# Performance work log

Measured on AMD Instinct MI355X. Metric: run time of the kernel, lower is better.

## Reference

```python
import jax, jax.numpy as jnp
import numpy as np


def setup_inputs() -> dict:
    key = jax.random.key(0)
    k1, k2, k3 = jax.random.split(key, 3)
    N, M, D, K = 8192, 8192, 512, 128
    x = jax.random.normal(k1, (N, D), dtype=jnp.float32)
    target = jax.random.normal(k2, (M, D), dtype=jnp.float32)
    W = jax.random.normal(k3, (D, K), dtype=jnp.float32) * 0.05
    return {"x": x, "target": target, "W": W}


def reference(x, target, W):
    # phi_Brenier(x): convex potential f(x) = logsumexp(x @ W)  -> [N]
    phi_b = jax.nn.logsumexp(x @ W, axis=-1)
    # phi_Kantorovich = 0.5||x||^2 - phi_Brenier  -> [N]
    x_sq = jnp.sum(x * x, axis=-1)
    phi_k = 0.5 * x_sq - phi_b
    t_sq = jnp.sum(target * target, axis=-1)
    DD = 0.5 * (x_sq[:, None] + t_sq[None, :] - 2.0 * (x @ target.T))
    # C-transform: min over source points  -> [M]
    phi_c = jnp.min(DD - phi_k[:, None], axis=0)
    # Kantorovich dual objective (scalar)
    return jnp.mean(phi_k) + jnp.mean(phi_c)
```

## Files before the change

### kernel.cpp

```cpp
#include <hip/hip_runtime.h>
#include <hip/hip_bf16.h>
#include <stdint.h>

typedef __attribute__((ext_vector_type(8))) short short8;
typedef __attribute__((ext_vector_type(4))) float f32x4;
typedef __attribute__((ext_vector_type(16))) float f32x16;
typedef __attribute__((ext_vector_type(4))) int i32x4;
typedef __attribute__((ext_vector_type(8))) int i32x8;

#define N_PTS 8192
#define M_PTS 8192
#define DIM   512
#define KDIM  128
#define BT    128
#define BKS   32

__device__ __forceinline__ unsigned fenc(float f) {
  unsigned u = __float_as_uint(f);
  return (u & 0x80000000u) ? ~u : (u | 0x80000000u);
}
__device__ __forceinline__ float fdec(unsigned k) {
  unsigned u = (k & 0x80000000u) ? (k ^ 0x80000000u) : ~k;
  return __uint_as_float(u);
}

__device__ __forceinline__ unsigned short f2bf(float f) {
  union { __hip_bfloat16 h; unsigned short u; } c;
  c.h = __float2bfloat16(f);
  return c.u;
}

__device__ __forceinline__ unsigned f2e4m3(float f) {
  unsigned u = __float_as_uint(f);
  unsigned s = (u >> 24) & 0x80;
  unsigned mag = u & 0x7fffffffu;
  unsigned r = mag + 0x0007ffffu + ((mag >> 20) & 1u);
  int e = (int)(r >> 23) - 127;
  if (e < -6) return s;
  unsigned m = (r >> 20) & 7u;
  return s | (unsigned)((e + 7) << 3) | m;
}

__device__ __forceinline__ void async_copy16(const void* g, void* l) {
  __builtin_amdgcn_global_load_lds(
      (const __attribute__((address_space(1))) void*)g,
      (__attribute__((address_space(3))) void*)l, 16, 0, 0);
}

__device__ __forceinline__ int swz_slot(int row, int slot) {
  return slot ^ ((row >> 1) & 3);
}

#define BARRIER __builtin_amdgcn_s_barrier()
#define LGKM0 do { asm volatile("s_waitcnt lgkmcnt(0)" ::: "memory"); \
                   __builtin_amdgcn_sched_barrier(0); } while (0)

__global__ __launch_bounds__(256)
void prep_all_kernel(const float* __restrict__ x, const float* __restrict__ tgt,
                     const float* __restrict__ W,
                     unsigned short* __restrict__ Xb, unsigned char* __restrict__ Xf8,
                     unsigned char* __restrict__ Tf8, unsigned short* __restrict__ WbT,
                     float* __restrict__ xsq, float* __restrict__ tsq,
                     unsigned* __restrict__ keys) {
  const int bid = blockIdx.x;
  const int tid = threadIdx.x;
  if (bid >= (N_PTS + M_PTS) / 4) {
    const int o = (bid - (N_PTS + M_PTS) / 4) * 256 + tid;
    const int k = o >> 9, d = o & 511;
    WbT[o] = f2bf(W[d * KDIM + k]);
    return;
  }
  const int gw = (bid * 256 + tid) >> 6;
  const int j = tid & 63;
  float s;
  if (gw < N_PTS) {
    const float* src = x + (size_t)gw * DIM + j * 8;
    float4 v0 = *(const float4*)src;
    float4 v1 = *(const float4*)(src + 4);
    s = v0.x * v0.x + v0.y * v0.y + v0.z * v0.z + v0.w * v0.w +
        v1.x * v1.x + v1.y * v1.y + v1.z * v1.z + v1.w * v1.w;
    unsigned short* db = Xb + (size_t)gw * DIM + j * 8;
    ushort4 ob0, ob1;
    ob0.x = f2bf(v0.x); ob0.y = f2bf(v0.y); ob0.z = f2bf(v0.z); ob0.w = f2bf(v0.w);
    ob1.x = f2bf(v1.x); ob1.y = f2bf(v1.y); ob1.z = f2bf(v1.z); ob1.w = f2bf(v1.w);
    *(ushort4*)db = ob0;
    *(ushort4*)(db + 4) = ob1;
    unsigned long long p = (unsigned long long)f2e4m3(v0.x)
        | ((unsigned long long)f2e4m3(v0.y) << 8)
        | ((unsigned long long)f2e4m3(v0.z) << 16)
        | ((unsigned long long)f2e4m3(v0.w) << 24)
        | ((unsigned long long)f2e4m3(v1.x) << 32)
        | ((unsigned long long)f2e4m3(v1.y) << 40)
        | ((unsigned long long)f2e4m3(v1.z) << 48)
        | ((unsigned long long)f2e4m3(v1.w) << 56);
    *(unsigned long long*)(Xf8 + (size_t)gw * DIM + j * 8) = p;
#pragma unroll
    for (int m = 1; m <= 32; m <<= 1) s += __shfl_xor(s, m);
    if (j == 0) xsq[gw] = s;
  } else {
    const int tr = gw - N_PTS;
    const float* src = tgt + (size_t)tr * DIM + j * 8;
    float4 v0 = *(const float4*)src;
    float4 v1 = *(const float4*)(src + 4);
    s = v0.x * v0.x + v0.y * v0.y + v0.z * v0.z + v0.w * v0.w +
        v1.x * v1.x + v1.y * v1.y + v1.z * v1.z + v1.w * v1.w;
    unsigned long long p = (unsigned long long)f2e4m3(v0.x)
        | ((unsigned long long)f2e4m3(v0.y) << 8)
        | ((unsigned long long)f2e4m3(v0.z) << 16)
        | ((unsigned long long)f2e4m3(v0.w) << 24)
        | ((unsigned long long)f2e4m3(v1.x) << 32)
        | ((unsigned long long)f2e4m3(v1.y) << 40)
        | ((unsigned long long)f2e4m3(v1.z) << 48)
        | ((unsigned long long)f2e4m3(v1.w) << 56);
    *(unsigned long long*)(Tf8 + (size_t)tr * DIM + j * 8) = p;
#pragma unroll
    for (int m = 1; m <= 32; m <<= 1) s += __shfl_xor(s, m);
    if (j == 0) { tsq[tr] = s; keys[tr] = 0xFFFFFFFFu; }
  }
}

__global__ __launch_bounds__(256)
void phi_b_kernel(const short* __restrict__ Xb, const short* __restrict__ WbT,
                  float* __restrict__ phi_b) {
  __shared__ __align__(16) short As[BT * BKS];
  __shared__ __align__(16) short Bs[BT * BKS];
  __shared__ __align__(16) float lg[128][136];

  const int tid = threadIdx.x;
  const int wave = tid >> 6, lane = tid & 63;
  const int n0 = blockIdx.x * BT;
  const int srow = tid >> 2;
  const int sk8 = swz_slot(srow, tid & 3) * 8;
  const int wr = wave >> 1, wc = wave & 1;
  const int fr = lane & 15, g = lane >> 4;

  f32x4 acc[4][4] = {};
  for (int kt = 0; kt < DIM / BKS; ++kt) {
    const int k0 = kt * BKS;
    async_copy16(Xb + (size_t)(n0 + srow) * DIM + k0 + sk8, &As[wave * 512]);
    async_copy16(Xb + (size_t)(n0 + srow + 64) * DIM + k0 + sk8, &As[2048 + wave * 512]);
    async_copy16(WbT + (size_t)srow * DIM + k0 + sk8, &Bs[wave * 512]);
    async_copy16(WbT + (size_t)(srow + 64) * DIM + k0 + sk8, &Bs[2048 + wave * 512]);
    __syncthreads();
    short8 a[4], b[4];
#pragma unroll
    for (int i = 0; i < 4; ++i) {
      const int R = wr * 64 + i * 16 + fr;
      a[i] = *(const short8*)&As[R * BKS + swz_slot(R, g) * 8];
    }
#pragma unroll
    for (int j = 0; j < 4; ++j) {
      const int R = wc * 64 + j * 16 + fr;
      b[j] = *(const short8*)&Bs[R * BKS + swz_slot(R, g) * 8];
    }
#pragma unroll
    for (int i = 0; i < 4; ++i)
#pragma unroll
      for (int j = 0; j < 4; ++j)
        acc[i][j] = __builtin_amdgcn_mfma_f32_16x16x32_bf16(a[i], b[j], acc[i][j], 0, 0, 0);
    __syncthreads();
  }

  const int rq = g * 4;
#pragma unroll
  for (int i = 0; i < 4; ++i)
#pragma unroll
    for (int j = 0; j < 4; ++j)
#pragma unroll
      for (int q = 0; q < 4; ++q)
        lg[wr * 64 + i * 16 + rq + q][wc * 64 + j * 16 + fr] = acc[i][j][q];
  __syncthreads();

  const int row = tid >> 1, half = tid & 1;
  const float4* lr = (const float4*)(&lg[row][half * 64]);
  float mx = -3.4e38f;
#pragma unroll
  for (int c = 0; c < 16; ++c) {
    float4 v = lr[c];
    mx = fmaxf(mx, fmaxf(fmaxf(v.x, v.y), fmaxf(v.z, v.w)));
  }
  mx = fmaxf(mx, __shfl_xor(mx, 1));
  float s = 0.f;
#pragma unroll
  for (int c = 0; c < 16; ++c) {
    float4 v = lr[c];
    s += __expf(v.x - mx) + __expf(v.y - mx) + __expf(v.z - mx) + __expf(v.w - mx);
  }
  s += __shfl_xor(s, 1);
  if (half == 0) phi_b[n0 + row] = mx + logf(s);
}

__device__ __forceinline__ void stg8(const unsigned char* __restrict__ mat,
                                     int rowbase, int kbyte,
                                     unsigned char* lds8, int dst, int tid) {
  const int r = tid >> 2, d = tid & 3;
  async_copy16(mat + (size_t)(rowbase + r) * DIM + kbyte + ((d ^ ((r >> 1) & 3)) << 4),
               lds8 + dst + (tid >> 6) * 1024);
}

__device__ __forceinline__ i32x8 ldfrag(const unsigned char* lds, int off) {
  i32x4 lo = *(const i32x4*)(lds + off);
  i32x4 hi = *(const i32x4*)(lds + (off ^ 16));
  return __builtin_shufflevector(lo, hi, 0, 1, 2, 3, 4, 5, 6, 7);
}

__device__ __forceinline__ f32x16 mfma_mx(i32x8 a, i32x8 b, f32x16 c) {
  return __builtin_amdgcn_mfma_scale_f32_32x32x64_f8f6f4(a, b, c, 0, 0,
                                                         0, 0x7F, 0, 0x7F);
}

template <int VMC, bool STG>
__device__ __forceinline__ void ktile_mx(unsigned char* lds8, int bufo,
                                         const unsigned char* __restrict__ Xf,
                                         const unsigned char* __restrict__ Tf,
                                         int n0, int m0, int kb2, int tid,
                                         int aoff, int boff, f32x16 (&acc)[4][2]) {
  const unsigned char* L = lds8 + bufo;
  i32x8 fa[4], fb[2];
#pragma unroll
  for (int i = 0; i < 4; ++i) fa[i] = ldfrag(L, aoff + i * 2048);
#pragma unroll
  for (int j = 0; j < 2; ++j) fb[j] = ldfrag(L, boff + j * 2048);
  BARRIER; LGKM0;
  __builtin_amdgcn_s_setprio(1);
#pragma unroll
  for (int i = 0; i < 4; ++i) acc[i][0] = mfma_mx(fa[i], fb[0], acc[i][0]);
  __builtin_amdgcn_s_setprio(0);
  BARRIER;
  if (STG) {
    stg8(Tf, m0, kb2, lds8, bufo + 16384, tid);
    stg8(Tf, m0 + 128, kb2, lds8, bufo + 16384 + 8192, tid);
    stg8(Xf, n0, kb2, lds8, bufo, tid);
    stg8(Xf, n0 + 128, kb2, lds8, bufo + 8192, tid);
  }
  __builtin_amdgcn_s_setprio(1);
#pragma unroll
  for (int i = 0; i < 4; ++i) acc[i][1] = mfma_mx(fa[i], fb[1], acc[i][1]);
  __builtin_amdgcn_s_setprio(0);
  if (VMC == 4) asm volatile("s_waitcnt vmcnt(4)" ::: "memory");
  else if (VMC == 0) asm volatile("s_waitcnt vmcnt(0)" ::: "memory");
  BARRIER;
}

__global__ __launch_bounds__(512, 2)
void gemm_min_kernel(const unsigned char* __restrict__ Xf, const unsigned char* __restrict__ Tf,
                     const float* __restrict__ phi_b, unsigned* __restrict__ keys) {
  __shared__ __align__(16) unsigned char lds8[65536];

  const int tid = threadIdx.x;
  const int wave = tid >> 6, lane = tid & 63;
  const int wm = wave >> 2, wn = wave & 3;
  const int fr5 = lane & 31, h = lane >> 5;

  const int bid = blockIdx.x;
  const int xcd = bid & 7, idx = bid >> 3;
  const int nt = (xcd >> 1) * 8 + (idx >> 4);
  const int mt = (xcd & 1) * 16 + (idx & 15);
  const int n0 = nt * 256, m0 = mt * 256;

  const int key = (fr5 >> 1) & 3;
  const int aoff = (wm * 128 + fr5) * 64 + (((h << 1) ^ key) << 4);
  const int boff = 16384 + (wn * 64 + fr5) * 64 + (((h << 1) ^ key) << 4);

  stg8(Tf, m0, 0, lds8, 16384, tid);
  stg8(Tf, m0 + 128, 0, lds8, 16384 + 8192, tid);
  stg8(Xf, n0, 0, lds8, 0, tid);
  stg8(Xf, n0 + 128, 0, lds8, 8192, tid);
  stg8(Tf, m0, 64, lds8, 32768 + 16384, tid);
  stg8(Tf, m0 + 128, 64, lds8, 32768 + 16384 + 8192, tid);
  stg8(Xf, n0, 64, lds8, 32768, tid);
  stg8(Xf, n0 + 128, 64, lds8, 32768 + 8192, tid);
  asm volatile("s_waitcnt vmcnt(4)" ::: "memory");
  BARRIER;

  f32x16 acc[4][2] = {};
#pragma unroll 1
  for (int t = 0; t < 6; ++t)
    ktile_mx<4, true>(lds8, (t & 1) * 32768, Xf, Tf, n0, m0, (t + 2) * 64,
                      tid, aoff, boff, acc);
  ktile_mx<0, false>(lds8, 0, Xf, Tf, n0, m0, 0, tid, aoff, boff, acc);
  ktile_mx<-1, false>(lds8, 32768, Xf, Tf, n0, m0, 0, tid, aoff, boff, acc);

  float mv0 = 3.4e38f, mv1 = 3.4e38f;
#pragma unroll
  for (int i = 0; i < 4; ++i) {
    float pb[16];
#pragma unroll
    for (int q = 0; q < 16; ++q)
      pb[q] = phi_b[n0 + wm * 128 + i * 32 + (q & 3) + 8 * (q >> 2) + 4 * h];
#pragma unroll
    for (int q = 0; q < 16; ++q) {
      mv0 = fminf(mv0, pb[q] - acc[i][0][q]);
      mv1 = fminf(mv1, pb[q] - acc[i][1][q]);
    }
  }
  mv0 = fminf(mv0, __shfl_xor(mv0, 32));
  mv1 = fminf(mv1, __shfl_xor(mv1, 32));
  if (h == 0) {
    atomicMin(&keys[m0 + wn * 64 + fr5], fenc(mv0));
    atomicMin(&keys[m0 + wn * 64 + 32 + fr5], fenc(mv1));
  }
}

__global__ __launch_bounds__(1024)
void finalize_kernel(const float* __restrict__ xsq, const float* __restrict__ phi_b,
                     const float* __restrict__ tsq, const unsigned* __restrict__ keys,
                     float* __restrict__ out) {
  const int t = threadIdx.x;
  double sk = 0.0, sc = 0.0;
  for (int n = t; n < N_PTS; n += 1024) sk += 0.5 * (double)xsq[n] - (double)phi_b[n];
  for (int m = t; m < M_PTS; m += 1024) sc += 0.5 * (double)tsq[m] + (double)fdec(keys[m]);
  const int lane = t & 63, wv = t >> 6;
#pragma unroll
  for (int m = 1; m <= 32; m <<= 1) {
    sk += __shfl_xor(sk, m);
    sc += __shfl_xor(sc, m);
  }
  __shared__ double pk[16], pc[16];
  if (lane == 0) { pk[wv] = sk; pc[wv] = sc; }
  __syncthreads();
  if (t == 0) {
    double a = 0.0, c = 0.0;
#pragma unroll
    for (int i = 0; i < 16; ++i) { a += pk[i]; c += pc[i]; }
    out[0] = (float)(a / N_PTS + c / M_PTS);
  }
}

extern "C" void kernel_launch(void* const* d_in, const int* in_sizes, int n_in,
                              void* d_out, int out_size, void* d_ws, size_t ws_size,
                              hipStream_t stream) {
  const float* x = (const float*)d_in[0];
  const float* tgt = (const float*)d_in[1];
  const float* W = (const float*)d_in[2];

  char* ws = (char*)d_ws;
  const size_t XB_BYTES = (size_t)N_PTS * DIM * 2;
  const size_t XF_BYTES = (size_t)N_PTS * DIM;
  const size_t TF_BYTES = (size_t)M_PTS * DIM;
  const size_t WT_BYTES = (size_t)KDIM * DIM * 2;
  unsigned short* Xb = (unsigned short*)ws;
  unsigned char* Xf8 = (unsigned char*)(ws + XB_BYTES);
  unsigned char* Tf8 = (unsigned char*)(ws + XB_BYTES + XF_BYTES);
  unsigned short* WbT = (unsigned short*)(ws + XB_BYTES + XF_BYTES + TF_BYTES);
  float* phi_b = (float*)(ws + XB_BYTES + XF_BYTES + TF_BYTES + WT_BYTES);
  float* xsq = phi_b + N_PTS;
  float* tsq = xsq + N_PTS;
  unsigned* keys = (unsigned*)(tsq + M_PTS);

  const int prep_blocks = (N_PTS + M_PTS) / 4 + (KDIM * DIM) / 256;
  prep_all_kernel<<<prep_blocks, 256, 0, stream>>>(x, tgt, W, Xb, Xf8, Tf8, WbT,
                                                   xsq, tsq, keys);
  phi_b_kernel<<<N_PTS / BT, 256, 0, stream>>>((const short*)Xb, (const short*)WbT, phi_b);
  gemm_min_kernel<<<(N_PTS / 256) * (M_PTS / 256), 512, 0, stream>>>(Xf8, Tf8, phi_b, keys);
  finalize_kernel<<<1, 1024, 0, stream>>>(xsq, phi_b, tsq, keys, (float*)d_out);
}
```

Before: 75.75 us.

## Load target fragments directly from global in k-blocked layout, triple-buffer X in LDS

The fp8 target matrix is stored in a k-tile-major layout so each wave can read its MFMA B fragments straight from global memory into registers, prefetched one k-tile ahead. Only X goes through LDS, now in a three-buffer ring, which removes one barrier per k-tile and cuts LDS use from 64KB to 48KB. The cost is more global-load latency on the critical path and redundant B reads across the two wm waves, with register pressure from the prefetched fragments. The wait counts are changed by hand to match the new number of outstanding loads.

Result: faster. 71.77 us (-5.3%).

```diff
diff --git a/kernel.cpp b/kernel.cpp
--- a/kernel.cpp
+++ b/kernel.cpp
@@ -52,14 +52,12 @@
 }
 
 #define BARRIER __builtin_amdgcn_s_barrier()
-#define LGKM0 do { asm volatile("s_waitcnt lgkmcnt(0)" ::: "memory"); \
-                   __builtin_amdgcn_sched_barrier(0); } while (0)
 
 __global__ __launch_bounds__(256)
 void prep_all_kernel(const float* __restrict__ x, const float* __restrict__ tgt,
                      const float* __restrict__ W,
                      unsigned short* __restrict__ Xb, unsigned char* __restrict__ Xf8,
-                     unsigned char* __restrict__ Tf8, unsigned short* __restrict__ WbT,
+                     unsigned char* __restrict__ TfT, unsigned short* __restrict__ WbT,
                      float* __restrict__ xsq, float* __restrict__ tsq,
                      unsigned* __restrict__ keys) {
   const int bid = blockIdx.x;
@@ -112,7 +110,7 @@
         | ((unsigned long long)f2e4m3(v1.y) << 40)
         | ((unsigned long long)f2e4m3(v1.z) << 48)
         | ((unsigned long long)f2e4m3(v1.w) << 56);
-    *(unsigned long long*)(Tf8 + (size_t)tr * DIM + j * 8) = p;
+    *(unsigned long long*)(TfT + ((size_t)(j >> 3) * M_PTS + tr) * 64 + (j & 7) * 8) = p;
 #pragma unroll
     for (int m = 1; m <= 32; m <<= 1) s += __shfl_xor(s, m);
     if (j == 0) { tsq[tr] = s; keys[tr] = 0xFFFFFFFFu; }
@@ -190,17 +188,17 @@
   if (half == 0) phi_b[n0 + row] = mx + logf(s);
 }
 
-__device__ __forceinline__ void stg8(const unsigned char* __restrict__ mat,
+__device__ __forceinline__ void stgA(const unsigned char* __restrict__ mat,
                                      int rowbase, int kbyte,
-                                     unsigned char* lds8, int dst, int tid) {
+                                     unsigned char* dst, int tid) {
   const int r = tid >> 2, d = tid & 3;
   async_copy16(mat + (size_t)(rowbase + r) * DIM + kbyte + ((d ^ ((r >> 1) & 3)) << 4),
-               lds8 + dst + (tid >> 6) * 1024);
-}
-
-__device__ __forceinline__ i32x8 ldfrag(const unsigned char* lds, int off) {
-  i32x4 lo = *(const i32x4*)(lds + off);
-  i32x4 hi = *(const i32x4*)(lds + (off ^ 16));
+               dst + (tid >> 6) * 1024);
+}
+
+__device__ __forceinline__ i32x8 ld2x16(const unsigned char* p0, const unsigned char* p1) {
+  i32x4 lo = *(const i32x4*)p0;
+  i32x4 hi = *(const i32x4*)p1;
   return __builtin_shufflevector(lo, hi, 0, 1, 2, 3, 4, 5, 6, 7);
 }
 
@@ -209,43 +207,41 @@
                                                          0, 0x7F, 0, 0x7F);
 }
 
-template <int VMC, bool STG>
-__device__ __forceinline__ void ktile_mx(unsigned char* lds8, int bufo,
-                                         const unsigned char* __restrict__ Xf,
-                                         const unsigned char* __restrict__ Tf,
-                                         int n0, int m0, int kb2, int tid,
-                                         int aoff, int boff, f32x16 (&acc)[4][2]) {
-  const unsigned char* L = lds8 + bufo;
-  i32x8 fa[4], fb[2];
-#pragma unroll
-  for (int i = 0; i < 4; ++i) fa[i] = ldfrag(L, aoff + i * 2048);
-#pragma unroll
-  for (int j = 0; j < 2; ++j) fb[j] = ldfrag(L, boff + j * 2048);
-  BARRIER; LGKM0;
+template <int VMC, bool STG, bool LDB, bool BAR>
+__device__ __forceinline__ void ktile(const unsigned char* Abuf, unsigned char* Sbuf,
+                                      const unsigned char* __restrict__ Xf,
+                                      const unsigned char* __restrict__ Bnx,
+                                      int n0, int kstage, int tid, int aoff,
+                                      i32x8 (&fb)[2], i32x8 (&fbn)[2],
+                                      f32x16 (&acc)[4][2]) {
+  i32x8 fa[4];
+#pragma unroll
+  for (int i = 0; i < 4; ++i)
+    fa[i] = ld2x16(Abuf + aoff + i * 2048, Abuf + ((aoff + i * 2048) ^ 16));
+  if (LDB) {
+    fbn[0] = ld2x16(Bnx, Bnx + 16);
+    fbn[1] = ld2x16(Bnx + 2048, Bnx + 2048 + 16);
+  }
+  if (STG) {
+    stgA(Xf, n0, kstage, Sbuf, tid);
+    stgA(Xf, n0 + 128, kstage, Sbuf + 8192, tid);
+  }
   __builtin_amdgcn_s_setprio(1);
 #pragma unroll
   for (int i = 0; i < 4; ++i) acc[i][0] = mfma_mx(fa[i], fb[0], acc[i][0]);
-  __builtin_amdgcn_s_setprio(0);
-  BARRIER;
-  if (STG) {
-    stg8(Tf, m0, kb2, lds8, bufo + 16384, tid);
-    stg8(Tf, m0 + 128, kb2, lds8, bufo + 16384 + 8192, tid);
-    stg8(Xf, n0, kb2, lds8, bufo, tid);
-    stg8(Xf, n0 + 128, kb2, lds8, bufo + 8192, tid);
-  }
-  __builtin_amdgcn_s_setprio(1);
 #pragma unroll
   for (int i = 0; i < 4; ++i) acc[i][1] = mfma_mx(fa[i], fb[1], acc[i][1]);
   __builtin_amdgcn_s_setprio(0);
-  if (VMC == 4) asm volatile("s_waitcnt vmcnt(4)" ::: "memory");
+  if (VMC == 6) asm volatile("s_waitcnt vmcnt(6)" ::: "memory");
+  else if (VMC == 4) asm volatile("s_waitcnt vmcnt(4)" ::: "memory");
   else if (VMC == 0) asm volatile("s_waitcnt vmcnt(0)" ::: "memory");
-  BARRIER;
+  if (BAR) BARRIER;
 }
 
 __global__ __launch_bounds__(512, 2)
-void gemm_min_kernel(const unsigned char* __restrict__ Xf, const unsigned char* __restrict__ Tf,
+void gemm_min_kernel(const unsigned char* __restrict__ Xf, const unsigned char* __restrict__ TfT,
                      const float* __restrict__ phi_b, unsigned* __restrict__ keys) {
-  __shared__ __align__(16) unsigned char lds8[65536];
+  __shared__ __align__(16) unsigned char lds8[49152];
 
   const int tid = threadIdx.x;
   const int wave = tid >> 6, lane = tid & 63;
@@ -260,26 +256,32 @@
 
   const int key = (fr5 >> 1) & 3;
   const int aoff = (wm * 128 + fr5) * 64 + (((h << 1) ^ key) << 4);
-  const int boff = 16384 + (wn * 64 + fr5) * 64 + (((h << 1) ^ key) << 4);
-
-  stg8(Tf, m0, 0, lds8, 16384, tid);
-  stg8(Tf, m0 + 128, 0, lds8, 16384 + 8192, tid);
-  stg8(Xf, n0, 0, lds8, 0, tid);
-  stg8(Xf, n0 + 128, 0, lds8, 8192, tid);
-  stg8(Tf, m0, 64, lds8, 32768 + 16384, tid);
-  stg8(Tf, m0 + 128, 64, lds8, 32768 + 16384 + 8192, tid);
-  stg8(Xf, n0, 64, lds8, 32768, tid);
-  stg8(Xf, n0 + 128, 64, lds8, 32768 + 8192, tid);
-  asm volatile("s_waitcnt vmcnt(4)" ::: "memory");
+
+  const unsigned char* Bb = TfT + ((size_t)(m0 + wn * 64 + fr5)) * 64 + h * 32;
+#define BK_T(kt) (Bb + (size_t)(kt) * (M_PTS * 64))
+
+  unsigned char* B0 = lds8;
+  unsigned char* B1 = lds8 + 16384;
+  unsigned char* B2 = lds8 + 32768;
+
+  stgA(Xf, n0, 0, B0, tid);       stgA(Xf, n0 + 128, 0, B0 + 8192, tid);
+  stgA(Xf, n0, 64, B1, tid);      stgA(Xf, n0 + 128, 64, B1 + 8192, tid);
+  asm volatile("s_waitcnt vmcnt(0)" ::: "memory");
   BARRIER;
 
+  i32x8 fbA[2], fbB[2];
+  fbA[0] = ld2x16(BK_T(0), BK_T(0) + 16);
+  fbA[1] = ld2x16(BK_T(0) + 2048, BK_T(0) + 2048 + 16);
+
   f32x16 acc[4][2] = {};
-#pragma unroll 1
-  for (int t = 0; t < 6; ++t)
-    ktile_mx<4, true>(lds8, (t & 1) * 32768, Xf, Tf, n0, m0, (t + 2) * 64,
-                      tid, aoff, boff, acc);
-  ktile_mx<0, false>(lds8, 0, Xf, Tf, n0, m0, 0, tid, aoff, boff, acc);
-  ktile_mx<-1, false>(lds8, 32768, Xf, Tf, n0, m0, 0, tid, aoff, boff, acc);
+  ktile<6, true, true, true>(B0, B2, Xf, BK_T(1), n0, 128, tid, aoff, fbA, fbB, acc);
+  ktile<6, true, true, true>(B1, B0, Xf, BK_T(2), n0, 192, tid, aoff, fbB, fbA, acc);
+  ktile<6, true, true, true>(B2, B1, Xf, BK_T(3), n0, 256, tid, aoff, fbA, fbB, acc);
+  ktile<6, true, true, true>(B0, B2, Xf, BK_T(4), n0, 320, tid, aoff, fbB, fbA, acc);
+  ktile<6, true, true, true>(B1, B0, Xf, BK_T(5), n0, 384, tid, aoff, fbA, fbB, acc);
+  ktile<6, true, true, true>(B2, B1, Xf, BK_T(6), n0, 448, tid, aoff, fbB, fbA, acc);
+  ktile<4, false, true, true>(B0, B2, Xf, BK_T(7), n0, 0, tid, aoff, fbA, fbB, acc);
+  ktile<-1, false, false, false>(B1, B2, Xf, BK_T(7), n0, 0, tid, aoff, fbB, fbA, acc);
 
   float mv0 = 3.4e38f, mv1 = 3.4e38f;
 #pragma unroll
@@ -300,6 +302,7 @@
     atomicMin(&keys[m0 + wn * 64 + fr5], fenc(mv0));
     atomicMin(&keys[m0 + wn * 64 + 32 + fr5], fenc(mv1));
   }
+#undef BK_T
 }
 
 __global__ __launch_bounds__(1024)
@@ -341,7 +344,7 @@
   const size_t WT_BYTES = (size_t)KDIM * DIM * 2;
   unsigned short* Xb = (unsigned short*)ws;
   unsigned char* Xf8 = (unsigned char*)(ws + XB_BYTES);
-  unsigned char* Tf8 = (unsigned char*)(ws + XB_BYTES + XF_BYTES);
+  unsigned char* TfT = (unsigned char*)(ws + XB_BYTES + XF_BYTES);
   unsigned short* WbT = (unsigned short*)(ws + XB_BYTES + XF_BYTES + TF_BYTES);
   float* phi_b = (float*)(ws + XB_BYTES + XF_BYTES + TF_BYTES + WT_BYTES);
   float* xsq = phi_b + N_PTS;
@@ -349,9 +352,9 @@
   unsigned* keys = (unsigned*)(tsq + M_PTS);
 
   const int prep_blocks = (N_PTS + M_PTS) / 4 + (KDIM * DIM) / 256;
-  prep_all_kernel<<<prep_blocks, 256, 0, stream>>>(x, tgt, W, Xb, Xf8, Tf8, WbT,
+  prep_all_kernel<<<prep_blocks, 256, 0, stream>>>(x, tgt, W, Xb, Xf8, TfT, WbT,
                                                    xsq, tsq, keys);
   phi_b_kernel<<<N_PTS / BT, 256, 0, stream>>>((const short*)Xb, (const short*)WbT, phi_b);
-  gemm_min_kernel<<<(N_PTS / 256) * (M_PTS / 256), 512, 0, stream>>>(Xf8, Tf8, phi_b, keys);
+  gemm_min_kernel<<<(N_PTS / 256) * (M_PTS / 256), 512, 0, stream>>>(Xf8, TfT, phi_b, keys);
   finalize_kernel<<<1, 1024, 0, stream>>>(xsq, phi_b, tsq, keys, (float*)d_out);
 }
```
